# Performance work log

Measured on AMD Instinct MI355X. Metric: run time of the kernel, lower is better.

## Reference

```python
import jax, jax.numpy as jnp
import numpy as np

TOPK_RATIO = 0.2
DICE_WEIGHT = 0.5
SHAPE = (2, 1, 128, 192, 192)


def setup_inputs() -> dict:
    key = jax.random.key(0)
    k1, k2 = jax.random.split(key)
    logits = jax.random.normal(k1, SHAPE, dtype=jnp.float32)
    targets = jax.random.uniform(k2, SHAPE, dtype=jnp.float32)
    return {"logits": logits, "targets": targets}


def _bce_with_logits(x, t):
    # stable: max(x,0) - x*t + log(1+exp(-|x|))
    return jnp.maximum(x, 0.0) - x * t + jnp.log1p(jnp.exp(-jnp.abs(x)))


def reference(logits, targets):
    # --- TopK BCE ---
    flat_loss = _bce_with_logits(logits, targets).reshape(-1)
    n = flat_loss.shape[0]
    k_samples = max(1, int(n * TOPK_RATIO))
    topk_losses, _ = jax.lax.top_k(flat_loss, k_samples)
    bce = jnp.mean(topk_losses)

    # --- Soft Dice ---
    p = jax.nn.sigmoid(logits).reshape(-1)
    t = targets.reshape(-1)
    intersection = jnp.sum(p * t)
    union = jnp.sum(p) + jnp.sum(t)
    dice = (2.0 * intersection + 1e-06) / (union + 1e-06)
    dice_loss = 1.0 - dice

    return bce + DICE_WEIGHT * dice_loss
```

## Files before the change

### kernel.cpp

```cpp
#include <hip/hip_runtime.h>
#include <math.h>
#include <limits.h>

#define NB1 8192
#define NB2 4096
#define VEC 4

__device__ __forceinline__ void elem_f(float x, float t, float& l, float& p) {
    float e = __expf(-fabsf(x));
    l = fmaxf(x, 0.f) - x * t + __logf(1.f + e);
    float r = __builtin_amdgcn_rcpf(1.f + e);
    p = (x >= 0.f) ? r : e * r;
}

__global__ __launch_bounds__(256) void sample_kernel(
    const float4* __restrict__ x4, const float4* __restrict__ t4,
    unsigned* __restrict__ H1, int n4)
{
    __shared__ unsigned lh[NB1];
    for (int i = threadIdx.x; i < NB1; i += 256) lh[i] = 0u;
    __syncthreads();

    int nth = gridDim.x * 256;
    int tid = blockIdx.x * 256 + threadIdx.x;
    int S4 = n4 >> 4;
    int i0 = tid, i1 = tid + nth;

    float4 xa, ta, xb, tb;
    bool v0 = i0 < S4, v1 = i1 < S4;
    if (v0) {
        int f4 = ((i0 >> 6) << 10) + (i0 & 63);
        xa = x4[f4]; ta = t4[f4];
    }
    if (v1) {
        int f4 = ((i1 >> 6) << 10) + (i1 & 63);
        xb = x4[f4]; tb = t4[f4];
    }
    if (v0) {
        float xs[4] = {xa.x, xa.y, xa.z, xa.w};
        float ts[4] = {ta.x, ta.y, ta.z, ta.w};
        #pragma unroll
        for (int c = 0; c < 4; ++c) {
            float l, p; elem_f(xs[c], ts[c], l, p);
            atomicAdd(&lh[__float_as_uint(l) >> 19], 1u);
        }
    }
    if (v1) {
        float xs[4] = {xb.x, xb.y, xb.z, xb.w};
        float ts[4] = {tb.x, tb.y, tb.z, tb.w};
        #pragma unroll
        for (int c = 0; c < 4; ++c) {
            float l, p; elem_f(xs[c], ts[c], l, p);
            atomicAdd(&lh[__float_as_uint(l) >> 19], 1u);
        }
    }
    __syncthreads();
    for (int i = threadIdx.x; i < NB1; i += 256) {
        unsigned c = lh[i];
        if (c) atomicAdd(&H1[i], c);
    }
}

__global__ __launch_bounds__(256) void band_kernel(
    const unsigned* __restrict__ H1, float* __restrict__ band,
    long long ks, long long M)
{
    __shared__ unsigned lh[NB1];
    const uint4* hv = (const uint4*)H1;
    uint4* lv = (uint4*)lh;
    for (int i = threadIdx.x; i < NB1 / 4; i += 256) lv[i] = hv[i];
    __syncthreads();
    if (threadIdx.x >= 64) return;

    int lane = threadIdx.x;
    int base = lane << 7;
    unsigned long long chunk = 0;
    for (int j = 0; j < 128; ++j) chunk += lh[base + j];
    unsigned long long s = chunk;
    #pragma unroll
    for (int off = 1; off < 64; off <<= 1) {
        unsigned long long v = __shfl_down(s, off);
        if (lane + off < 64) s += v;
    }
    unsigned long long above = s - chunk;

    int my_bhi = INT_MAX, my_blo = -1;
    unsigned long long c = above;
    for (int j = 127; j >= 0; --j) {
        unsigned h = lh[base + j];
        if ((long long)(c + h) < ks - M) my_bhi = base + j;
        if ((long long)c > ks + M && my_blo < 0) my_blo = base + j;
        c += h;
    }
    #pragma unroll
    for (int off = 32; off; off >>= 1) {
        int a = __shfl_down(my_bhi, off); my_bhi = min(my_bhi, a);
        int b = __shfl_down(my_blo, off); my_blo = max(my_blo, b);
    }
    if (lane == 0) {
        int bhi = (my_bhi == INT_MAX) ? (NB1 - 1) : my_bhi;
        int blo = my_blo;
        float vhi = __uint_as_float((unsigned)bhi << 19);
        float vlo = (blo < 0) ? 0.f : __uint_as_float((unsigned)(blo + 1) << 19);
        if (!(vlo < vhi)) vlo = 0.f;
        band[0] = vlo;
        band[1] = vhi;
    }
}

__device__ __forceinline__ void process4(
    float4 xv, float4 tv, float vlo, float vhi, float scale,
    float& sp, float& spt, float& st, float& sgt, unsigned& cnt,
    unsigned* __restrict__ hist2)
{
    float xs[4] = {xv.x, xv.y, xv.z, xv.w};
    float ts[4] = {tv.x, tv.y, tv.z, tv.w};
    #pragma unroll
    for (int c = 0; c < 4; ++c) {
        float l, p;
        elem_f(xs[c], ts[c], l, p);
        sp += p; spt += p * ts[c]; st += ts[c];
        if (l >= vhi) { cnt++; sgt += l; }
        else if (l >= vlo) {
            int b = min((int)((l - vlo) * scale), NB2 - 1);
            atomicAdd(&hist2[b], 1u);
        }
    }
}

__global__ __launch_bounds__(256, 4) void main_kernel(
    const float4* __restrict__ x4, const float4* __restrict__ t4,
    const float* __restrict__ band, unsigned* __restrict__ hist2,
    float* __restrict__ q0, float* __restrict__ q1,
    float* __restrict__ q2, float* __restrict__ q3, unsigned* __restrict__ qc,
    const float* __restrict__ xg, const float* __restrict__ tg,
    int n, int n4)
{
    float vlo = band[0], vhi = band[1];
    float scale = (float)NB2 / (vhi - vlo);

    int base = blockIdx.x * (256 * VEC) + threadIdx.x;
    float sp = 0.f, spt = 0.f, st = 0.f, sgt = 0.f;
    unsigned cnt = 0;

    bool full = (blockIdx.x + 1) * (256 * VEC) <= n4;
    if (full) {
        float4 xv[VEC], tv[VEC];
        #pragma unroll
        for (int j = 0; j < VEC; ++j) xv[j] = x4[base + j * 256];
        #pragma unroll
        for (int j = 0; j < VEC; ++j) tv[j] = t4[base + j * 256];
        #pragma unroll
        for (int j = 0; j < VEC; ++j)
            process4(xv[j], tv[j], vlo, vhi, scale, sp, spt, st, sgt, cnt, hist2);
    } else {
        for (int j = 0; j < VEC; ++j) {
            int idx = base + j * 256;
            if (idx < n4)
                process4(x4[idx], t4[idx], vlo, vhi, scale, sp, spt, st, sgt, cnt, hist2);
        }
    }
    int tail0 = n4 << 2;
    if (blockIdx.x == 0 && threadIdx.x < (n - tail0)) {
        float x = xg[tail0 + threadIdx.x], t = tg[tail0 + threadIdx.x];
        float l, p;
        elem_f(x, t, l, p);
        sp += p; spt += p * t; st += t;
        if (l >= vhi) { cnt++; sgt += l; }
        else if (l >= vlo) {
            int b = min((int)((l - vlo) * scale), NB2 - 1);
            atomicAdd(&hist2[b], 1u);
        }
    }

    #pragma unroll
    for (int off = 32; off; off >>= 1) {
        sp  += __shfl_down(sp,  off);
        spt += __shfl_down(spt, off);
        st  += __shfl_down(st,  off);
        sgt += __shfl_down(sgt, off);
        cnt += __shfl_down(cnt, off);
    }
    __shared__ float    rs[4][4];
    __shared__ unsigned rc[4];
    int w = threadIdx.x >> 6;
    if ((threadIdx.x & 63) == 0) {
        rs[w][0] = sp; rs[w][1] = spt; rs[w][2] = st; rs[w][3] = sgt; rc[w] = cnt;
    }
    __syncthreads();
    if (threadIdx.x == 0) {
        float a0 = 0, a1 = 0, a2 = 0, a3 = 0;
        unsigned c = 0;
        #pragma unroll
        for (int i = 0; i < 4; ++i) {
            a0 += rs[i][0]; a1 += rs[i][1]; a2 += rs[i][2]; a3 += rs[i][3]; c += rc[i];
        }
        q0[blockIdx.x] = a0; q1[blockIdx.x] = a1; q2[blockIdx.x] = a2;
        q3[blockIdx.x] = a3; qc[blockIdx.x] = c;
    }
}

__global__ __launch_bounds__(1024) void final_kernel(
    const unsigned* __restrict__ hist2, const float* __restrict__ band,
    const float* __restrict__ q0, const float* __restrict__ q1,
    const float* __restrict__ q2, const float* __restrict__ q3,
    const unsigned* __restrict__ qc, int nblocks,
    float* __restrict__ out, long long k)
{
    __shared__ unsigned lh[NB2];
    __shared__ double red[16][5];
    __shared__ double fin[5];

    for (int i = threadIdx.x; i < NB2; i += 1024) lh[i] = hist2[i];

    double a0 = 0, a1 = 0, a2 = 0, a3 = 0, a4 = 0;
    for (int i = threadIdx.x; i < nblocks; i += 1024) {
        a0 += (double)q0[i]; a1 += (double)q1[i]; a2 += (double)q2[i];
        a3 += (double)q3[i]; a4 += (double)qc[i];
    }
    #pragma unroll
    for (int off = 32; off; off >>= 1) {
        a0 += __shfl_down(a0, off); a1 += __shfl_down(a1, off);
        a2 += __shfl_down(a2, off); a3 += __shfl_down(a3, off);
        a4 += __shfl_down(a4, off);
    }
    int w = threadIdx.x >> 6;
    if ((threadIdx.x & 63) == 0) {
        red[w][0] = a0; red[w][1] = a1; red[w][2] = a2; red[w][3] = a3; red[w][4] = a4;
    }
    __syncthreads();
    if (threadIdx.x == 0) {
        double f0 = 0, f1 = 0, f2 = 0, f3 = 0, f4 = 0;
        for (int i = 0; i < 16; ++i) {
            f0 += red[i][0]; f1 += red[i][1]; f2 += red[i][2];
            f3 += red[i][3]; f4 += red[i][4];
        }
        fin[0] = f0; fin[1] = f1; fin[2] = f2; fin[3] = f3; fin[4] = f4;
    }
    __syncthreads();
    if (threadIdx.x >= 64) return;

    int lane = threadIdx.x;
    double SP = fin[0], SPT = fin[1], ST = fin[2], SGT = fin[3];
    long long CNT = (long long)fin[4];

    double vlo = (double)band[0], vhi = (double)band[1];
    double binw = (vhi - vlo) / NB2;
    long long k2 = k - CNT;

    int base = lane << 6;
    unsigned long long cchunk = 0;
    double wchunk = 0.0;
    for (int j = 0; j < 64; ++j) {
        unsigned h = lh[base + j];
        cchunk += h;
        wchunk += (double)h * (vlo + (base + j + 0.5) * binw);
    }
    unsigned long long cs = cchunk;
    double wsum = wchunk;
    #pragma unroll
    for (int off = 1; off < 64; off <<= 1) {
        unsigned long long cv = __shfl_down(cs, off);
        double wv = __shfl_down(wsum, off);
        if (lane + off < 64) { cs += cv; wsum += wv; }
    }
    unsigned long long total = __shfl(cs, 0);
    double wtotal = __shfl(wsum, 0);

    double I = SPT, U = SP + ST;
    double dice_part = 0.5 * (1.0 - (2.0 * I + 1e-6) / (U + 1e-6));

    if (k2 <= 0) {
        if (lane == 0) out[0] = (float)(SGT / (double)k + dice_part);
        return;
    }
    if ((unsigned long long)k2 > total) {
        if (lane == 0) {
            double sum_top = SGT + wtotal + (double)(k2 - (long long)total) * vlo;
            out[0] = (float)(sum_top / (double)k + dice_part);
        }
        return;
    }
    unsigned long long c = cs - cchunk;
    double wacc = wsum - wchunk;
    for (int j = 63; j >= 0; --j) {
        unsigned h = lh[base + j];
        double val = vlo + (base + j + 0.5) * binw;
        if (c < (unsigned long long)k2 && (unsigned long long)k2 <= c + h) {
            double sum_top = SGT + wacc + (double)((long long)k2 - (long long)c) * val;
            out[0] = (float)(sum_top / (double)k + dice_part);
        }
        c += h;
        wacc += (double)h * val;
    }
}

extern "C" void kernel_launch(void* const* d_in, const int* in_sizes, int n_in,
                              void* d_out, int out_size, void* d_ws, size_t ws_size,
                              hipStream_t stream)
{
    const float* x = (const float*)d_in[0];
    const float* t = (const float*)d_in[1];
    float* out = (float*)d_out;
    int n = in_sizes[0];
    int n4 = n >> 2;
    long long k = (long long)((double)n * 0.2);
    if (k < 1) k = 1;

    long long S = (long long)(n4 >> 4) * 4;
    long long ks = (S > 0) ? (long long)((double)k * (double)S / (double)n) : 0;
    long long M = 4096;

    int tilesz = 256 * VEC;
    int grid = (n4 + tilesz - 1) / tilesz;
    if (grid < 1) grid = 1;

    int S4 = n4 >> 4;
    int sgrid = (S4 + 511) / 512;
    if (sgrid < 1) sgrid = 1;

    unsigned char* ws = (unsigned char*)d_ws;
    unsigned* H1    = (unsigned*)(ws);
    unsigned* hist2 = (unsigned*)(ws + 32768);
    float*    band  = (float*)(ws + 49152);
    size_t po = 50176;
    size_t pstride = (((size_t)grid * 4) + 255) & ~(size_t)255;
    float*    q0 = (float*)(ws + po);
    float*    q1 = (float*)(ws + po + pstride);
    float*    q2 = (float*)(ws + po + 2 * pstride);
    float*    q3 = (float*)(ws + po + 3 * pstride);
    unsigned* qc = (unsigned*)(ws + po + 4 * pstride);

    hipMemsetAsync(d_ws, 0, 49152, stream);

    sample_kernel<<<sgrid, 256, 0, stream>>>((const float4*)x, (const float4*)t, H1, n4);
    band_kernel<<<1, 256, 0, stream>>>(H1, band, ks, M);
    main_kernel<<<grid, 256, 0, stream>>>((const float4*)x, (const float4*)t,
                                          band, hist2, q0, q1, q2, q3, qc, x, t, n, n4);
    final_kernel<<<1, 1024, 0, stream>>>(hist2, band, q0, q1, q2, q3, qc, grid, out, k);
}
```

Baseline: 138.4 us.

## Privatize band histogram in LDS and double per-thread work in main kernel

In the main pass, band-histogram updates now go to a per-block shared-memory histogram that is flushed to global memory with one atomic per non-empty bin, where each element previously hit a global atomic. VEC rises from 4 to 8, halving the main grid, and the global loads are issued before the LDS-zeroing barrier so memory latency overlaps the initialisation. The sample kernel now gives one float4 per thread over twice as many blocks and likewise moves its barrier after the loads. The cost is a 16 KB LDS histogram per main block plus its zero/flush work, and more registers with the looser launch bounds, which may reduce occupancy.

After: 144.9 us. 4.7% more time.

```diff
diff --git a/kernel.cpp b/kernel.cpp
--- a/kernel.cpp
+++ b/kernel.cpp
@@ -4,7 +4,7 @@
 
 #define NB1 8192
 #define NB2 4096
-#define VEC 4
+#define VEC 8
 
 __device__ __forceinline__ void elem_f(float x, float t, float& l, float& p) {
     float e = __expf(-fabsf(x));
@@ -19,35 +19,19 @@
 {
     __shared__ unsigned lh[NB1];
     for (int i = threadIdx.x; i < NB1; i += 256) lh[i] = 0u;
-    __syncthreads();
-
-    int nth = gridDim.x * 256;
+
     int tid = blockIdx.x * 256 + threadIdx.x;
     int S4 = n4 >> 4;
-    int i0 = tid, i1 = tid + nth;
-
-    float4 xa, ta, xb, tb;
-    bool v0 = i0 < S4, v1 = i1 < S4;
-    if (v0) {
-        int f4 = ((i0 >> 6) << 10) + (i0 & 63);
+    bool v = tid < S4;
+    float4 xa, ta;
+    if (v) {
+        int f4 = ((tid >> 6) << 10) + (tid & 63);
         xa = x4[f4]; ta = t4[f4];
     }
-    if (v1) {
-        int f4 = ((i1 >> 6) << 10) + (i1 & 63);
-        xb = x4[f4]; tb = t4[f4];
-    }
-    if (v0) {
+    __syncthreads();
+    if (v) {
         float xs[4] = {xa.x, xa.y, xa.z, xa.w};
         float ts[4] = {ta.x, ta.y, ta.z, ta.w};
-        #pragma unroll
-        for (int c = 0; c < 4; ++c) {
-            float l, p; elem_f(xs[c], ts[c], l, p);
-            atomicAdd(&lh[__float_as_uint(l) >> 19], 1u);
-        }
-    }
-    if (v1) {
-        float xs[4] = {xb.x, xb.y, xb.z, xb.w};
-        float ts[4] = {tb.x, tb.y, tb.z, tb.w};
         #pragma unroll
         for (int c = 0; c < 4; ++c) {
             float l, p; elem_f(xs[c], ts[c], l, p);
@@ -108,27 +92,7 @@
     }
 }
 
-__device__ __forceinline__ void process4(
-    float4 xv, float4 tv, float vlo, float vhi, float scale,
-    float& sp, float& spt, float& st, float& sgt, unsigned& cnt,
-    unsigned* __restrict__ hist2)
-{
-    float xs[4] = {xv.x, xv.y, xv.z, xv.w};
-    float ts[4] = {tv.x, tv.y, tv.z, tv.w};
-    #pragma unroll
-    for (int c = 0; c < 4; ++c) {
-        float l, p;
-        elem_f(xs[c], ts[c], l, p);
-        sp += p; spt += p * ts[c]; st += ts[c];
-        if (l >= vhi) { cnt++; sgt += l; }
-        else if (l >= vlo) {
-            int b = min((int)((l - vlo) * scale), NB2 - 1);
-            atomicAdd(&hist2[b], 1u);
-        }
-    }
-}
-
-__global__ __launch_bounds__(256, 4) void main_kernel(
+__global__ __launch_bounds__(256) void main_kernel(
     const float4* __restrict__ x4, const float4* __restrict__ t4,
     const float* __restrict__ band, unsigned* __restrict__ hist2,
     float* __restrict__ q0, float* __restrict__ q1,
@@ -136,28 +100,62 @@
     const float* __restrict__ xg, const float* __restrict__ tg,
     int n, int n4)
 {
+    __shared__ unsigned lh2[NB2];
+    for (int i = threadIdx.x; i < NB2; i += 256) lh2[i] = 0u;
+
     float vlo = band[0], vhi = band[1];
     float scale = (float)NB2 / (vhi - vlo);
 
     int base = blockIdx.x * (256 * VEC) + threadIdx.x;
+    bool full = (blockIdx.x + 1) * (256 * VEC) <= n4;
+
+    float4 xv[VEC], tv[VEC];
+    if (full) {
+        #pragma unroll
+        for (int j = 0; j < VEC; ++j) xv[j] = x4[base + j * 256];
+        #pragma unroll
+        for (int j = 0; j < VEC; ++j) tv[j] = t4[base + j * 256];
+    }
+    __syncthreads();
+
     float sp = 0.f, spt = 0.f, st = 0.f, sgt = 0.f;
     unsigned cnt = 0;
 
-    bool full = (blockIdx.x + 1) * (256 * VEC) <= n4;
     if (full) {
-        float4 xv[VEC], tv[VEC];
-        #pragma unroll
-        for (int j = 0; j < VEC; ++j) xv[j] = x4[base + j * 256];
-        #pragma unroll
-        for (int j = 0; j < VEC; ++j) tv[j] = t4[base + j * 256];
-        #pragma unroll
-        for (int j = 0; j < VEC; ++j)
-            process4(xv[j], tv[j], vlo, vhi, scale, sp, spt, st, sgt, cnt, hist2);
+        #pragma unroll
+        for (int j = 0; j < VEC; ++j) {
+            float xs[4] = {xv[j].x, xv[j].y, xv[j].z, xv[j].w};
+            float ts[4] = {tv[j].x, tv[j].y, tv[j].z, tv[j].w};
+            #pragma unroll
+            for (int c = 0; c < 4; ++c) {
+                float l, p;
+                elem_f(xs[c], ts[c], l, p);
+                sp += p; spt += p * ts[c]; st += ts[c];
+                if (l >= vhi) { cnt++; sgt += l; }
+                else if (l >= vlo) {
+                    int b = min((int)((l - vlo) * scale), NB2 - 1);
+                    atomicAdd(&lh2[b], 1u);
+                }
+            }
+        }
     } else {
         for (int j = 0; j < VEC; ++j) {
             int idx = base + j * 256;
-            if (idx < n4)
-                process4(x4[idx], t4[idx], vlo, vhi, scale, sp, spt, st, sgt, cnt, hist2);
+            if (idx >= n4) continue;
+            float4 xq = x4[idx], tq = t4[idx];
+            float xs[4] = {xq.x, xq.y, xq.z, xq.w};
+            float ts[4] = {tq.x, tq.y, tq.z, tq.w};
+            #pragma unroll
+            for (int c = 0; c < 4; ++c) {
+                float l, p;
+                elem_f(xs[c], ts[c], l, p);
+                sp += p; spt += p * ts[c]; st += ts[c];
+                if (l >= vhi) { cnt++; sgt += l; }
+                else if (l >= vlo) {
+                    int b = min((int)((l - vlo) * scale), NB2 - 1);
+                    atomicAdd(&lh2[b], 1u);
+                }
+            }
         }
     }
     int tail0 = n4 << 2;
@@ -169,8 +167,14 @@
         if (l >= vhi) { cnt++; sgt += l; }
         else if (l >= vlo) {
             int b = min((int)((l - vlo) * scale), NB2 - 1);
-            atomicAdd(&hist2[b], 1u);
-        }
+            atomicAdd(&lh2[b], 1u);
+        }
+    }
+
+    __syncthreads();
+    for (int i = threadIdx.x; i < NB2; i += 256) {
+        unsigned c = lh2[i];
+        if (c) atomicAdd(&hist2[i], c);
     }
 
     #pragma unroll
@@ -316,7 +320,7 @@
     if (grid < 1) grid = 1;
 
     int S4 = n4 >> 4;
-    int sgrid = (S4 + 511) / 512;
+    int sgrid = (S4 + 255) / 256;
     if (sgrid < 1) sgrid = 1;
 
     unsigned char* ws = (unsigned char*)d_ws;
```
